# Optimization experiments

Hardware: AMD Instinct MI355X
Metric: run time of the kernel (lower is better)

## Reference

```python
import jax, jax.numpy as jnp
import numpy as np
import math

M, N, D = 16384, 8192, 128
SIGMA = 1.0

def setup_inputs() -> dict:
    key = jax.random.key(0)
    k1, k2, k3 = jax.random.split(key, 3)
    x = jax.random.normal(k1, (M, D), dtype=jnp.float32)
    means = jax.random.normal(k2, (N, D), dtype=jnp.float32)
    weights = jax.random.uniform(k3, (N,), dtype=jnp.float32)
    return {"x": x, "means": means, "weights": weights}

def reference(x, means, weights):
    # GMM.eval_batch: cdist -> square -> gaussian kernel -> weighted sum
    var = SIGMA ** 2
    x = x.reshape(-1, means.shape[-1])
    x2 = jnp.sum(x * x, axis=-1, keepdims=True)            # (M,1)
    m2 = jnp.sum(means * means, axis=-1)                   # (N,)
    sq = jnp.maximum(x2 + m2[None, :] - 2.0 * (x @ means.T), 0.0)  # (M,N)
    coef = 1.0 / (2.0 * math.pi * var)
    dens = coef * jnp.exp(-sq / (2.0 * var))               # (M,N)
    return dens @ weights                                  # (M,)
```

## Files before the change

### kernel.cpp

```cpp
#include <hip/hip_runtime.h>
#include <math.h>

#define MM 16384
#define NN 8192
#define DD 128

#define L2E  1.4426950408889634f
#define COEF 0.15915494309189535f

__device__ __forceinline__ unsigned short f2h(float f) {
    _Float16 h = (_Float16)f;
    unsigned short u;
    __builtin_memcpy(&u, &h, 2);
    return u;
}

__device__ __forceinline__ void async16(short* lds, const short* g) {
    __builtin_amdgcn_global_load_lds(
        (const __attribute__((address_space(1))) unsigned int*)g,
        (__attribute__((address_space(3))) unsigned int*)lds,
        16, 0, 0);
}

typedef __attribute__((ext_vector_type(8))) _Float16 f16x8;
typedef __attribute__((ext_vector_type(4))) float f32x4;

__global__ __launch_bounds__(256) void gmm_prep_f16(
    const float* __restrict__ x, const float* __restrict__ means,
    const float* __restrict__ w, short* __restrict__ Acat,
    short* __restrict__ Bcat, float* __restrict__ xc, float* __restrict__ mc)
{
    const int tid  = threadIdx.x;
    const int rbk  = blockIdx.x;
    const bool isx = rbk < (MM / 16);
    const int rb   = isx ? rbk : rbk - (MM / 16);
    const int lane = tid & 63;
    const int rp   = (tid >> 6) * 4 + (lane >> 4);
    const int cg   = lane & 15;
    const int p    = cg >> 2;
    const int gk   = cg & 3;
    const int row  = rb * 16 + rp;

    const float* src = (isx ? x : means) + (size_t)row * DD + cg * 8;
    float4 u0 = ((const float4*)src)[0];
    float4 u1 = ((const float4*)src)[1];
    float a[8] = {u0.x, u0.y, u0.z, u0.w, u1.x, u1.y, u1.z, u1.w};

    float ss = 0.f;
    unsigned hi[4];
    #pragma unroll
    for (int q = 0; q < 4; ++q) {
        ss = fmaf(a[2 * q], a[2 * q], fmaf(a[2 * q + 1], a[2 * q + 1], ss));
        float a0 = isx ? a[2 * q] * L2E     : a[2 * q];
        float a1 = isx ? a[2 * q + 1] * L2E : a[2 * q + 1];
        hi[q] = (unsigned)f2h(a0) | ((unsigned)f2h(a1) << 16);
    }
    uint4 HI = make_uint4(hi[0], hi[1], hi[2], hi[3]);

    const int slot = rp * 4 + ((gk + (rp >> 1)) & 3);
    short* base = (isx ? Acat : Bcat) + (size_t)rb * 2048 + p * 512 + slot * 8;
    *(uint4*)base = HI;

    ss += __shfl_xor(ss, 1, 16);
    ss += __shfl_xor(ss, 2, 16);
    ss += __shfl_xor(ss, 4, 16);
    ss += __shfl_xor(ss, 8, 16);
    if (cg == 0) {
        if (isx) xc[row] = -0.5f * ss * L2E;
        else     mc[row] = (logf(w[row]) - 0.5f * ss) * L2E;
    }
}

__global__ __launch_bounds__(512, 3) void gmm_mfma(
    const short* __restrict__ Acat, const short* __restrict__ Bcat,
    const float* __restrict__ xc, const float* __restrict__ mc,
    float* __restrict__ out)
{
    __shared__ __align__(16) short smem[24576];
    __shared__ float red[4][128];

#define AS(b) (smem + (b) * 4096)
#define BS(b) (smem + 8192 + (b) * 8192)

    const int tid  = threadIdx.x;
    const int w    = tid >> 6, lane = tid & 63;
    const int wm   = w >> 2,   wn   = w & 3;
    const int quad = lane >> 4, col = lane & 15;
    const int m0   = blockIdx.x * 128;
    const int nb   = blockIdx.y * 256;

    const short* ga  = Acat + (size_t)(blockIdx.x * 8 + w) * 2048 + lane * 8;
    const short* gb0 = Bcat + (size_t)(blockIdx.y * 16 + w * 2) * 2048 + lane * 8;
    const short* gb1 = gb0 + 2048;
    const int aofs  = w * 512;
    const int bofs0 = w * 1024;
    const int bofs1 = w * 1024 + 512;

    float mcv[4];
    #pragma unroll
    for (int j = 0; j < 4; ++j) mcv[j] = mc[nb + wn * 64 + j * 16 + col];
    float xa[4][4];
    #pragma unroll
    for (int i = 0; i < 4; ++i) {
        float4 xv = *(const float4*)(xc + m0 + wm * 64 + i * 16 + quad * 4);
        xa[i][0] = xv.x; xa[i][1] = xv.y; xa[i][2] = xv.z; xa[i][3] = xv.w;
    }

    async16(AS(0) + aofs,  ga);
    async16(BS(0) + bofs0, gb0);
    async16(BS(0) + bofs1, gb1);

    f32x4 acc[4][4];
    #pragma unroll
    for (int i = 0; i < 4; ++i)
        #pragma unroll
        for (int j = 0; j < 4; ++j)
            acc[i][j] = (f32x4){xa[i][0] + mcv[j], xa[i][1] + mcv[j],
                                xa[i][2] + mcv[j], xa[i][3] + mcv[j]};

    const int rdo = col * 32 + ((quad + (col >> 1)) & 3) * 8;

    #pragma unroll 1
    for (int bk = 0; bk < 4; ++bk) {
        __syncthreads();
        if (bk < 3) {
            async16(AS((bk + 1) & 1) + aofs,  ga  + (bk + 1) * 512);
            async16(BS((bk + 1) & 1) + bofs0, gb0 + (bk + 1) * 512);
            async16(BS((bk + 1) & 1) + bofs1, gb1 + (bk + 1) * 512);
        }
        const short* as = AS(bk & 1);
        const short* bs = BS(bk & 1);
        f16x8 af[4];
        #pragma unroll
        for (int i = 0; i < 4; ++i)
            af[i] = *(const f16x8*)(as + (wm * 4 + i) * 512 + rdo);
        #pragma unroll
        for (int j = 0; j < 4; ++j) {
            f16x8 bfr = *(const f16x8*)(&bs[(wn * 4 + j) * 512 + rdo]);
            #pragma unroll
            for (int i = 0; i < 4; ++i)
                acc[i][j] = __builtin_amdgcn_mfma_f32_16x16x32_f16(
                    af[i], bfr, acc[i][j], 0, 0, 0);
        }
    }

    float sv[4][4];
    #pragma unroll
    for (int i = 0; i < 4; ++i) {
        #pragma unroll
        for (int r = 0; r < 4; ++r) {
            float s = 0.f;
            #pragma unroll
            for (int j = 0; j < 4; ++j)
                s += __builtin_exp2f(acc[i][j][r]);
            sv[i][r] = s;
        }
    }
    __syncthreads();
    {
        float* S = (float*)smem;
        const int p = wn * 16 + col;
        #pragma unroll
        for (int i = 0; i < 4; ++i) {
            const int mb = wm * 64 + i * 16 + quad * 4;
            #pragma unroll
            for (int r = 0; r < 4; ++r)
                S[(mb + r) * 68 + p] = sv[i][r];
        }
    }
    __syncthreads();
    {
        const float* S = (const float*)smem;
        const int m  = tid & 127;
        const int pg = tid >> 7;
        const float4* v = (const float4*)(S + m * 68 + pg * 16);
        float4 a0 = v[0], a1 = v[1], a2 = v[2], a3 = v[3];
        red[pg][m] = (a0.x + a0.y + a0.z + a0.w) + (a1.x + a1.y + a1.z + a1.w)
                   + (a2.x + a2.y + a2.z + a2.w) + (a3.x + a3.y + a3.z + a3.w);
    }
    __syncthreads();
    if (tid < 128)
        atomicAdd(out + m0 + tid,
                  COEF * (red[0][tid] + red[1][tid] + red[2][tid] + red[3][tid]));
#undef AS
#undef BS
}

__global__ __launch_bounds__(256) void gmm_prep(
    const float* __restrict__ x, const float* __restrict__ means,
    const float* __restrict__ w, float* __restrict__ xc, float* __restrict__ mc)
{
    int tid = blockIdx.x * 256 + threadIdx.x;
    if (tid < MM) {
        const float4* row = (const float4*)(x + (size_t)tid * DD);
        float ss = 0.f;
        #pragma unroll
        for (int i = 0; i < DD / 4; ++i) {
            float4 v = row[i];
            ss = fmaf(v.x, v.x, fmaf(v.y, v.y, fmaf(v.z, v.z, fmaf(v.w, v.w, ss))));
        }
        xc[tid] = -0.5f * ss * L2E;
    } else if (tid < MM + NN) {
        int n = tid - MM;
        const float4* row = (const float4*)(means + (size_t)n * DD);
        float ss = 0.f;
        #pragma unroll
        for (int i = 0; i < DD / 4; ++i) {
            float4 v = row[i];
            ss = fmaf(v.x, v.x, fmaf(v.y, v.y, fmaf(v.z, v.z, fmaf(v.w, v.w, ss))));
        }
        mc[n] = (logf(w[n]) - 0.5f * ss) * L2E;
    }
}

__global__ __launch_bounds__(256, 2) void gmm_main(
    const float* __restrict__ x, const float* __restrict__ means,
    const float* __restrict__ xc, const float* __restrict__ mc,
    float* __restrict__ out)
{
    __shared__ __align__(16) float Asm[128 * 128];
    __shared__ __align__(16) float Bsm[2][16 * 128];

    const int t   = threadIdx.x;
    const int tc  = t & 15;
    const int tr  = t >> 4;
    const int r0  = blockIdx.x * 128;
    const int nq0 = blockIdx.y * 2048;

    {
        float4 tmp[16];
        #pragma unroll
        for (int ii = 0; ii < 16; ++ii) {
            int idx = t + ii * 256;
            int r   = idx >> 5;
            int k0  = (idx & 31) << 2;
            tmp[ii] = *(const float4*)(x + (size_t)(r0 + r) * DD + k0);
        }
        #pragma unroll
        for (int ii = 0; ii < 16; ++ii) {
            int idx = t + ii * 256;
            int r   = idx >> 5;
            int k0  = (idx & 31) << 2;
            int rb  = r >> 3, rl = r & 7;
            float v[4] = {tmp[ii].x, tmp[ii].y, tmp[ii].z, tmp[ii].w};
            #pragma unroll
            for (int j = 0; j < 4; ++j) {
                int k = k0 + j;
                Asm[k * 128 + (((rb ^ (k & 15)) << 3) | rl)] = v[j];
            }
        }
    }

    float xcv[8];
    {
        float4 a = *(const float4*)(xc + r0 + tr * 8);
        float4 b = *(const float4*)(xc + r0 + tr * 8 + 4);
        xcv[0] = a.x; xcv[1] = a.y; xcv[2] = a.z; xcv[3] = a.w;
        xcv[4] = b.x; xcv[5] = b.y; xcv[6] = b.z; xcv[7] = b.w;
    }

    float rowAcc[8];
    #pragma unroll
    for (int i = 0; i < 8; ++i) rowAcc[i] = 0.f;

    for (int ntile = 0; ntile < 16; ++ntile) {
        const int nbase = nq0 + ntile * 128;

        float acc[8][8];
        #pragma unroll
        for (int i = 0; i < 8; ++i)
            #pragma unroll
            for (int j = 0; j < 8; ++j) acc[i][j] = 0.f;

        float4 ld[2];
        #pragma unroll
        for (int ii = 0; ii < 2; ++ii) {
            int flat = t + ii * 256;
            int nl   = flat >> 2;
            int kl   = (flat & 3) << 2;
            ld[ii] = *(const float4*)(means + (size_t)(nbase + nl) * DD + kl);
        }

        for (int ks = 0; ks < 8; ++ks) {
            const int buf = ks & 1;
            #pragma unroll
            for (int ii = 0; ii < 2; ++ii) {
                int flat = t + ii * 256;
                int nl   = flat >> 2;
                int k0   = (flat & 3) << 2;
                int nbk  = nl >> 3, nll = nl & 7;
                float v[4] = {ld[ii].x, ld[ii].y, ld[ii].z, ld[ii].w};
                #pragma unroll
                for (int j = 0; j < 4; ++j) {
                    int kl = k0 + j;
                    Bsm[buf][kl * 128 + (((nbk ^ kl) << 3) | nll)] = v[j];
                }
            }
            if (ks < 7) {
                #pragma unroll
                for (int ii = 0; ii < 2; ++ii) {
                    int flat = t + ii * 256;
                    int nl   = flat >> 2;
                    int kl   = (flat & 3) << 2;
                    ld[ii] = *(const float4*)(means + (size_t)(nbase + nl) * DD
                                              + (ks + 1) * 16 + kl);
                }
            }
            __syncthreads();

            #pragma unroll
            for (int kk = 0; kk < 16; ++kk) {
                const int k = ks * 16 + kk;
                const float* apx = &Asm[k * 128 + ((tr ^ kk) << 3)];
                float4 a0 = *(const float4*)apx;
                float4 a1 = *(const float4*)(apx + 4);
                const float* bpx = &Bsm[buf][kk * 128 + ((tc ^ kk) << 3)];
                float4 b0 = *(const float4*)bpx;
                float4 b1 = *(const float4*)(bpx + 4);
                float av[8] = {a0.x, a0.y, a0.z, a0.w, a1.x, a1.y, a1.z, a1.w};
                float bv[8] = {b0.x, b0.y, b0.z, b0.w, b1.x, b1.y, b1.z, b1.w};
                #pragma unroll
                for (int i = 0; i < 8; ++i)
                    #pragma unroll
                    for (int j = 0; j < 8; ++j)
                        acc[i][j] = fmaf(av[i], bv[j], acc[i][j]);
            }
        }

        float mcv[8];
        {
            float4 a = *(const float4*)(mc + nbase + tc * 8);
            float4 b = *(const float4*)(mc + nbase + tc * 8 + 4);
            mcv[0] = a.x; mcv[1] = a.y; mcv[2] = a.z; mcv[3] = a.w;
            mcv[4] = b.x; mcv[5] = b.y; mcv[6] = b.z; mcv[7] = b.w;
        }
        #pragma unroll
        for (int i = 0; i < 8; ++i) {
            float s = 0.f;
            #pragma unroll
            for (int j = 0; j < 8; ++j) {
                float arg = fmaf(acc[i][j], L2E, xcv[i] + mcv[j]);
                s += __builtin_exp2f(arg);
            }
            rowAcc[i] += s;
        }
    }

    #pragma unroll
    for (int i = 0; i < 8; ++i) {
        float v = rowAcc[i];
        v += __shfl_xor(v, 1, 16);
        v += __shfl_xor(v, 2, 16);
        v += __shfl_xor(v, 4, 16);
        v += __shfl_xor(v, 8, 16);
        if (tc == 0) atomicAdd(out + r0 + tr * 8 + i, COEF * v);
    }
}

extern "C" void kernel_launch(void* const* d_in, const int* in_sizes, int n_in,
                              void* d_out, int out_size, void* d_ws, size_t ws_size,
                              hipStream_t stream) {
    const float* x     = (const float*)d_in[0];
    const float* means = (const float*)d_in[1];
    const float* w     = (const float*)d_in[2];
    float* out = (float*)d_out;

    const size_t needA = (size_t)MM * 128 * sizeof(short);
    const size_t needB = (size_t)NN * 128 * sizeof(short);
    const size_t need  = needA + needB + (size_t)(MM + NN) * 4;

    if (ws_size >= need) {
        short* Acat = (short*)d_ws;
        short* Bcat = Acat + (size_t)MM * 128;
        float* xc   = (float*)(Bcat + (size_t)NN * 128);
        float* mc   = xc + MM;
        hipMemsetAsync(out, 0, MM * sizeof(float), stream);
        gmm_prep_f16<<<(MM + NN) / 16, 256, 0, stream>>>(x, means, w, Acat, Bcat, xc, mc);
        gmm_mfma<<<dim3(MM / 128, NN / 256), 512, 0, stream>>>(Acat, Bcat, xc, mc, out);
    } else {
        float* xc = (float*)d_ws;
        float* mc = xc + MM;
        hipMemsetAsync(out, 0, MM * sizeof(float), stream);
        gmm_prep<<<(MM + NN + 255) / 256, 256, 0, stream>>>(x, means, w, xc, mc);
        gmm_main<<<dim3(MM / 128, 4), 256, 0, stream>>>(x, means, xc, mc, out);
    }
}
```

Before: 126.1 us.

## Load MFMA operands directly from global memory into registers, dropping LDS staging

The GEMM main loop no longer stages A/B tiles through LDS with async global-to-LDS copies and per-step barriers. Each wave now reads its pre-swizzled fp16 fragments straight from global memory into registers, double-buffering two k-steps in software and raising wave priority around MFMA bursts. This removes the LDS round trip and three barriers per block, and shrinks LDS to the reduction buffer, which could allow more resident blocks. The trade-off is that waves sharing a row or column tile now load the same fragments redundantly from global/L2, and register pressure rises from holding two operand sets.

Result: slower. 136.0 us (+7.9%).

```diff
diff --git a/kernel.cpp b/kernel.cpp
--- a/kernel.cpp
+++ b/kernel.cpp
@@ -13,13 +13,6 @@
     unsigned short u;
     __builtin_memcpy(&u, &h, 2);
     return u;
-}
-
-__device__ __forceinline__ void async16(short* lds, const short* g) {
-    __builtin_amdgcn_global_load_lds(
-        (const __attribute__((address_space(1))) unsigned int*)g,
-        (__attribute__((address_space(3))) unsigned int*)lds,
-        16, 0, 0);
 }
 
 typedef __attribute__((ext_vector_type(8))) _Float16 f16x8;
@@ -76,11 +69,8 @@
     const float* __restrict__ xc, const float* __restrict__ mc,
     float* __restrict__ out)
 {
-    __shared__ __align__(16) short smem[24576];
+    __shared__ __align__(16) float S[128 * 68];
     __shared__ float red[4][128];
-
-#define AS(b) (smem + (b) * 4096)
-#define BS(b) (smem + 8192 + (b) * 8192)
 
     const int tid  = threadIdx.x;
     const int w    = tid >> 6, lane = tid & 63;
@@ -89,12 +79,10 @@
     const int m0   = blockIdx.x * 128;
     const int nb   = blockIdx.y * 256;
 
-    const short* ga  = Acat + (size_t)(blockIdx.x * 8 + w) * 2048 + lane * 8;
-    const short* gb0 = Bcat + (size_t)(blockIdx.y * 16 + w * 2) * 2048 + lane * 8;
-    const short* gb1 = gb0 + 2048;
-    const int aofs  = w * 512;
-    const int bofs0 = w * 1024;
-    const int bofs1 = w * 1024 + 512;
+    const int rdo = col * 32 + ((quad + (col >> 1)) & 3) * 8;
+
+    const short* ga = Acat + (size_t)(blockIdx.x * 8 + wm * 4) * 2048 + rdo;
+    const short* gb = Bcat + (size_t)(blockIdx.y * 16 + wn * 4) * 2048 + rdo;
 
     float mcv[4];
     #pragma unroll
@@ -106,10 +94,6 @@
         xa[i][0] = xv.x; xa[i][1] = xv.y; xa[i][2] = xv.z; xa[i][3] = xv.w;
     }
 
-    async16(AS(0) + aofs,  ga);
-    async16(BS(0) + bofs0, gb0);
-    async16(BS(0) + bofs1, gb1);
-
     f32x4 acc[4][4];
     #pragma unroll
     for (int i = 0; i < 4; ++i)
@@ -118,31 +102,38 @@
             acc[i][j] = (f32x4){xa[i][0] + mcv[j], xa[i][1] + mcv[j],
                                 xa[i][2] + mcv[j], xa[i][3] + mcv[j]};
 
-    const int rdo = col * 32 + ((quad + (col >> 1)) & 3) * 8;
-
-    #pragma unroll 1
-    for (int bk = 0; bk < 4; ++bk) {
-        __syncthreads();
-        if (bk < 3) {
-            async16(AS((bk + 1) & 1) + aofs,  ga  + (bk + 1) * 512);
-            async16(BS((bk + 1) & 1) + bofs0, gb0 + (bk + 1) * 512);
-            async16(BS((bk + 1) & 1) + bofs1, gb1 + (bk + 1) * 512);
-        }
-        const short* as = AS(bk & 1);
-        const short* bs = BS(bk & 1);
-        f16x8 af[4];
-        #pragma unroll
-        for (int i = 0; i < 4; ++i)
-            af[i] = *(const f16x8*)(as + (wm * 4 + i) * 512 + rdo);
-        #pragma unroll
-        for (int j = 0; j < 4; ++j) {
-            f16x8 bfr = *(const f16x8*)(&bs[(wn * 4 + j) * 512 + rdo]);
-            #pragma unroll
-            for (int i = 0; i < 4; ++i)
-                acc[i][j] = __builtin_amdgcn_mfma_f32_16x16x32_f16(
-                    af[i], bfr, acc[i][j], 0, 0, 0);
-        }
-    }
+#define LOADSET(A_, B_, OFS)                                                  \
+    {                                                                         \
+        _Pragma("unroll")                                                     \
+        for (int i = 0; i < 4; ++i)                                           \
+            A_[i] = *(const f16x8*)(ga + (size_t)i * 2048 + (OFS));           \
+        _Pragma("unroll")                                                     \
+        for (int j = 0; j < 4; ++j)                                           \
+            B_[j] = *(const f16x8*)(gb + (size_t)j * 2048 + (OFS));           \
+    }
+#define MFMASET(A_, B_)                                                       \
+    {                                                                         \
+        __builtin_amdgcn_s_setprio(1);                                        \
+        _Pragma("unroll")                                                     \
+        for (int j = 0; j < 4; ++j)                                           \
+            _Pragma("unroll")                                                 \
+            for (int i = 0; i < 4; ++i)                                       \
+                acc[i][j] = __builtin_amdgcn_mfma_f32_16x16x32_f16(           \
+                    A_[i], B_[j], acc[i][j], 0, 0, 0);                        \
+        __builtin_amdgcn_s_setprio(0);                                        \
+    }
+
+    f16x8 fa0[4], fb0[4], fa1[4], fb1[4];
+    LOADSET(fa0, fb0, 0);
+    LOADSET(fa1, fb1, 512);
+    MFMASET(fa0, fb0);
+    LOADSET(fa0, fb0, 1024);
+    MFMASET(fa1, fb1);
+    LOADSET(fa1, fb1, 1536);
+    MFMASET(fa0, fb0);
+    MFMASET(fa1, fb1);
+#undef LOADSET
+#undef MFMASET
 
     float sv[4][4];
     #pragma unroll
@@ -156,21 +147,18 @@
             sv[i][r] = s;
         }
     }
+    {
+        const int p = wn * 16 + col;
+        #pragma unroll
+        for (int i = 0; i < 4; ++i) {
+            const int mb = wm * 64 + i * 16 + quad * 4;
+            #pragma unroll
+            for (int r = 0; r < 4; ++r)
+                S[(mb + r) * 68 + p] = sv[i][r];
+        }
+    }
     __syncthreads();
     {
-        float* S = (float*)smem;
-        const int p = wn * 16 + col;
-        #pragma unroll
-        for (int i = 0; i < 4; ++i) {
-            const int mb = wm * 64 + i * 16 + quad * 4;
-            #pragma unroll
-            for (int r = 0; r < 4; ++r)
-                S[(mb + r) * 68 + p] = sv[i][r];
-        }
-    }
-    __syncthreads();
-    {
-        const float* S = (const float*)smem;
         const int m  = tid & 127;
         const int pg = tid >> 7;
         const float4* v = (const float4*)(S + m * 68 + pg * 16);
@@ -182,8 +170,6 @@
     if (tid < 128)
         atomicAdd(out + m0 + tid,
                   COEF * (red[0][tid] + red[1][tid] + red[2][tid] + red[3][tid]));
-#undef AS
-#undef BS
 }
 
 __global__ __launch_bounds__(256) void gmm_prep(
```
